# Optimization experiments

Measured on AMD Instinct MI355X. Metric: run time of the kernel, lower is better.

The kernel has to match this reference:

```python
import jax, jax.numpy as jnp
import numpy as np
import math

DIM = 128
HEAD = 4
RANK = 32
HEAD_DIM = DIM // HEAD
B, T, N, F = 2, 128, 1024, 128  # t == f == dim required by the original module
EXPAND = 4
EPS = 1e-6


def setup_inputs() -> dict:
    key = jax.random.key(0)
    ks = jax.random.split(key, 12)
    s = 0.02
    return {
        "x": jax.random.normal(ks[0], (B, T, N, F), jnp.float32),
        "norm_w": jnp.ones((DIM,), jnp.float32),
        "q_w": jax.random.normal(ks[1], (DIM, DIM), jnp.float32) * s,   # (out,in)
        "q_b": jnp.zeros((DIM,), jnp.float32),
        "key_p": jax.random.normal(ks[2], (RANK, HEAD, HEAD_DIM), jnp.float32),
        "v_w": jax.random.normal(ks[3], (DIM, DIM), jnp.float32) * s,
        "v_b": jnp.zeros((DIM,), jnp.float32),
        "alpha": jnp.full((HEAD, 1), math.log(9.0), jnp.float32),
        "beta": jnp.full((HEAD, 1), math.log(0.01), jnp.float32),
        "w1": jax.random.normal(ks[4], (EXPAND * DIM, DIM), jnp.float32) * s,
        "b1": jnp.zeros((EXPAND * DIM,), jnp.float32),
        "w2": jax.random.normal(ks[5], (EXPAND * DIM, DIM), jnp.float32) * s,
        "b2": jnp.zeros((EXPAND * DIM,), jnp.float32),
        "w3": jax.random.normal(ks[6], (DIM, EXPAND * DIM), jnp.float32) * s,
        "b3": jnp.zeros((DIM,), jnp.float32),
    }


def _rmsnorm(x, w):
    # NOTE: original reduces over axis 1 (the t axis), weight broadcasts on last axis
    var = jnp.mean(x * x, axis=1, keepdims=True)
    return w * (x * jax.lax.rsqrt(var + EPS))


def _attention(x, q_w, q_b, key_p, v_w, v_b, alpha, beta):
    b, t, n, f = x.shape
    q = (jnp.einsum('btnf,of->btno', x, q_w) + q_b).reshape(b, t, n, HEAD, HEAD_DIM)
    attn = jnp.einsum('btnhd,rhd->btnhr', q, key_p) / (HEAD_DIM ** 0.5)
    xv = (jnp.einsum('btnf,of->btno', x, v_w) + v_b).reshape(b, t, n, HEAD, HEAD_DIM)
    # softmax over rank, aggregate values into landmarks
    v = jnp.einsum('btnhr,btnhd->btrhd', jax.nn.softmax(attn, axis=-1), xv)
    # softmax over node axis (axis=-3 of btnhr), scatter landmarks back to nodes
    v = jnp.einsum('btnhr,btrhd->btnhd', jax.nn.softmax(attn, axis=-3), v)
    v = jax.nn.sigmoid(alpha) * xv + jax.nn.sigmoid(beta) * v
    return v.reshape(b, t, n, f)


def _conv1x1(x, w, b):
    # Conv2d kernel_size=1 on (B, C=t, H=n, W=f)
    return jnp.einsum('oc,bcnf->bonf', w, x) + b[None, :, None, None]


def _ffn(x, w1, b1, w2, b2, w3, b3):
    h = jax.nn.silu(_conv1x1(x, w1, b1)) * _conv1x1(x, w2, b2)
    return _conv1x1(h, w3, b3)  # dropout is identity in eval mode


def reference(x, norm_w, q_w, q_b, key_p, v_w, v_b, alpha, beta,
              w1, b1, w2, b2, w3, b3):
    x = _attention(_rmsnorm(x, norm_w), q_w, q_b, key_p, v_w, v_b, alpha, beta) + x
    x = _ffn(_rmsnorm(x, norm_w), w1, b1, w2, b2, w3, b3) + x
    return x
```

## Files before the change

kernel.cpp:

```cpp
#include <hip/hip_runtime.h>

#define DEV static __device__ __forceinline__

constexpr int Bc = 2, Tc = 128, Nc = 1024, Fc = 128, Hc = 4, Rc = 32, Dc = 32;
constexpr int NF  = Nc * Fc;
constexpr int TOK = Bc * Tc * Nc;
constexpr float EPSc = 1e-6f;
constexpr float RSD  = 0.17677669529663687f;

typedef __bf16 bf16x8 __attribute__((ext_vector_type(8)));
typedef float  f32x16 __attribute__((ext_vector_type(16)));
typedef unsigned short us8 __attribute__((ext_vector_type(8)));
typedef unsigned short us4 __attribute__((ext_vector_type(4)));

DEV unsigned short f2bu(float f) {
    unsigned u = __builtin_bit_cast(unsigned, f);
    u += 0x7fffu + ((u >> 16) & 1u);
    return (unsigned short)(u >> 16);
}
DEV float bu2f(unsigned short s) {
    return __builtin_bit_cast(float, ((unsigned)s) << 16);
}
DEV float sigmoidf_(float z) { return 1.f / (1.f + __expf(-z)); }
DEV f32x16 zero16() { f32x16 z;
#pragma unroll
    for (int i = 0; i < 16; i++) z[i] = 0.f;
    return z; }

__global__ void k_prep(const float* __restrict__ q_w, const float* __restrict__ q_b,
                       const float* __restrict__ key_p, const float* __restrict__ v_b,
                       const float* __restrict__ v_w,
                       unsigned short* __restrict__ Wcat, float* __restrict__ bias,
                       const float* __restrict__ w1, const float* __restrict__ w2,
                       const float* __restrict__ w3, unsigned short* __restrict__ wbf)
{
    __shared__ float sqw[32][128];
    __shared__ float skp[32][32];
    const int blk = blockIdx.x, tid = threadIdx.x;
    if (blk < 4) {
        int h = blk;
        for (int i = tid; i < 4096; i += 256) {
            int d = i >> 7, c = i & 127;
            sqw[d][c] = q_w[(size_t)(h * 32 + d) * 128 + c];
        }
        for (int i = tid; i < 1024; i += 256) {
            int r = i >> 5, d = i & 31;
            skp[r][d] = key_p[(size_t)(r * 4 + h) * 32 + d] * RSD;
        }
        __syncthreads();
        int r = tid >> 3;
        int c0 = (tid & 7) * 16;
        for (int cc = 0; cc < 16; ++cc) {
            int c = c0 + cc;
            float s = 0.f;
#pragma unroll
            for (int d = 0; d < 32; ++d) s = fmaf(sqw[d][c], skp[r][d], s);
            Wcat[(size_t)(h * 32 + r) * 128 + c] = f2bu(s);
        }
        if (tid < 32) {
            float s = 0.f;
#pragma unroll
            for (int d = 0; d < 32; ++d) s = fmaf(q_b[h * 32 + d], skp[tid][d], s);
            bias[h * 32 + tid] = s;
        }
        if (h == 0 && tid >= 64 && tid < 192) bias[128 + tid - 64] = v_b[tid - 64];
        return;
    }
    const float* src;
    unsigned short* dst;
    long i8;
    if (blk < 12) {
        i8 = (long)(blk - 4) * 2048 + tid * 8;
        src = v_w; dst = Wcat + 16384;
    } else {
        i8 = (long)(blk - 12) * 2048 + tid * 8;
        if (i8 < 65536)        { src = w1; dst = wbf; }
        else if (i8 < 131072)  { src = w2 - 65536; dst = wbf; }
        else                   { src = w3 - 131072; dst = wbf; }
    }
    float4 u0 = *(const float4*)(src + i8);
    float4 u1 = *(const float4*)(src + i8 + 4);
    us4 p0, p1;
    p0[0] = f2bu(u0.x); p0[1] = f2bu(u0.y); p0[2] = f2bu(u0.z); p0[3] = f2bu(u0.w);
    p1[0] = f2bu(u1.x); p1[1] = f2bu(u1.y); p1[2] = f2bu(u1.z); p1[3] = f2bu(u1.w);
    *(us4*)(dst + i8)     = p0;
    *(us4*)(dst + i8 + 4) = p1;
}

constexpr int XPF = 132;
__global__ __launch_bounds__(256, 2) void k_projm(
    const float* __restrict__ x, const float* __restrict__ nw,
    const unsigned short* __restrict__ Wcat, const float* __restrict__ bias,
    unsigned short* __restrict__ Lb, unsigned short* __restrict__ XVb)
{
    __shared__ float xs[128 * XPF];
    __shared__ float sscale[128];
    const int tid = threadIdx.x, lane = tid & 63, wv = tid >> 6;
    const int lr = lane & 31, lhi = lane >> 5;
    const int blk = blockIdx.x;
    const int b = blk >> 10, n = blk & 1023;

    const float* xg = x + ((size_t)(b * Tc) * Nc + n) * 128;
#pragma unroll
    for (int p = 0; p < 8; ++p) {
        int i = p * 256 + tid;
        int t = i >> 4, cg = i & 15;
        const float* src = xg + (size_t)t * NF + cg * 8;
        float4 u0 = *(const float4*)src;
        float4 u1 = *(const float4*)(src + 4);
        int col = t ^ ((cg & 7) << 3);
        float vv[8] = {u0.x, u0.y, u0.z, u0.w, u1.x, u1.y, u1.z, u1.w};
#pragma unroll
        for (int j = 0; j < 8; ++j) xs[(cg * 8 + j) * XPF + col] = vv[j];
    }
    __syncthreads();

    {
        int c = tid >> 1, half = tid & 1;
        float ss = 0.f;
#pragma unroll
        for (int k = 0; k < 16; ++k) {
            float4 u = *(const float4*)&xs[c * XPF + half * 64 + k * 4];
            ss = fmaf(u.x, u.x, fmaf(u.y, u.y, fmaf(u.z, u.z, fmaf(u.w, u.w, ss))));
        }
        ss += __shfl_xor(ss, 1);
        if (half == 0) sscale[c] = rsqrtf(ss * (1.f / Tc) + EPSc) * nw[c];
    }
    __syncthreads();

    bf16x8 af[8];
#pragma unroll
    for (int s = 0; s < 8; ++s) {
        const int cbase = s * 16 + lhi * 8;
        const int col = (wv * 32 + lr) ^ (((cbase >> 3) & 7) << 3);
        bf16x8 v;
#pragma unroll
        for (int j = 0; j < 8; ++j) {
            const int c = cbase + j;
            v[j] = (__bf16)(xs[c * XPF + col] * sscale[c]);
        }
        af[s] = v;
    }

#pragma unroll
    for (int ot = 0; ot < 8; ++ot) {
        const unsigned short* pw = Wcat + (size_t)(ot * 32 + lr) * 128 + lhi * 8;
        f32x16 acc = zero16();
#pragma unroll
        for (int s = 0; s < 8; ++s) {
            bf16x8 bw = *(const bf16x8*)(pw + s * 16);
            acc = __builtin_amdgcn_mfma_f32_32x32x16_bf16(af[s], bw, acc, 0, 0, 0);
        }
        const int o = ot * 32 + lr;
        const float bv = bias[o];
        unsigned short* dst = (ot < 4) ? Lb : XVb;
        const int oo = (ot < 4) ? o : o - 128;
#pragma unroll
        for (int r = 0; r < 16; ++r) {
            const int t = wv * 32 + (r & 3) + 8 * (r >> 2) + 4 * lhi;
            dst[((size_t)(b * Tc + t) * Nc + n) * 128 + oo] = f2bu(acc[r] + bv);
        }
    }
}

__global__ __launch_bounds__(256, 4) void k_land(
    const unsigned short* __restrict__ Lb, const unsigned short* __restrict__ XVb,
    float* __restrict__ VL, float* __restrict__ M2, float* __restrict__ S2)
{
    __shared__ float sL [64][34];
    __shared__ float sXV[64][36];
    __shared__ float redm[32][8];
    __shared__ float reds[32][8];
    int tid = threadIdx.x;
    int blk = blockIdx.x;
    int h = blk & 3; int bt = blk >> 2;
    size_t base = (size_t)bt * Nc * 128 + h * 32;
    const int li = tid >> 2, c8 = (tid & 3) * 8;
    const int r_st = tid & 31, stripe = tid >> 5;
    const int ti = tid >> 2, sub = tid & 3;
    const int r_acc = tid >> 3, d0 = (tid & 7) * 4;
    float m_st = -1e30f, s_st = 0.f;
    float a0 = 0, a1 = 0, a2 = 0, a3 = 0;
    for (int n0 = 0; n0 < Nc; n0 += 64) {
        {
            size_t g = base + (size_t)(n0 + li) * 128 + c8;
            us8 vL = *(const us8*)(Lb + g);
            us8 vX = *(const us8*)(XVb + g);
#pragma unroll
            for (int j = 0; j < 8; ++j) {
                sL [li][c8 + j] = bu2f(vL[j]);
                sXV[li][c8 + j] = bu2f(vX[j]);
            }
        }
        __syncthreads();
#pragma unroll
        for (int i8 = 0; i8 < 8; ++i8) {
            float v = sL[stripe * 8 + i8][r_st];
            float mn = fmaxf(m_st, v);
            s_st = s_st * __expf(m_st - mn) + __expf(v - mn);
            m_st = mn;
        }
        float e[8];
        float mx = -1e30f;
#pragma unroll
        for (int j = 0; j < 8; ++j) mx = fmaxf(mx, sL[ti][sub * 8 + j]);
        mx = fmaxf(mx, __shfl_xor(mx, 1));
        mx = fmaxf(mx, __shfl_xor(mx, 2));
        float sm = 0.f;
#pragma unroll
        for (int j = 0; j < 8; ++j) { e[j] = __expf(sL[ti][sub * 8 + j] - mx); sm += e[j]; }
        sm += __shfl_xor(sm, 1);
        sm += __shfl_xor(sm, 2);
        float iv = 1.f / sm;
        __syncthreads();
#pragma unroll
        for (int j = 0; j < 8; ++j) sL[ti][sub * 8 + j] = e[j] * iv;
        __syncthreads();
#pragma unroll 2
        for (int i = 0; i < 64; ++i) {
            float p = sL[i][r_acc];
            float4 v = *(const float4*)&sXV[i][d0];
            a0 = fmaf(p, v.x, a0); a1 = fmaf(p, v.y, a1);
            a2 = fmaf(p, v.z, a2); a3 = fmaf(p, v.w, a3);
        }
        __syncthreads();
    }
    redm[r_st][stripe] = m_st;
    reds[r_st][stripe] = s_st;
    __syncthreads();
    if (tid < 32) {
        float m = -1e30f;
#pragma unroll
        for (int k = 0; k < 8; ++k) m = fmaxf(m, redm[tid][k]);
        float s = 0.f;
#pragma unroll
        for (int k = 0; k < 8; ++k) s += reds[tid][k] * __expf(redm[tid][k] - m);
        M2[blk * 32 + tid] = m;
        S2[blk * 32 + tid] = s;
    }
    *(float4*)&VL[((size_t)blk * 32 + r_acc) * 32 + d0] = make_float4(a0, a1, a2, a3);
}

__global__ __launch_bounds__(256) void k_out1(
    const float* __restrict__ x,
    const unsigned short* __restrict__ Lb, const unsigned short* __restrict__ XVb,
    const float* __restrict__ VL, const float* __restrict__ M2, const float* __restrict__ S2,
    const float* __restrict__ alpha, const float* __restrict__ beta,
    unsigned short* __restrict__ X2b)
{
    __shared__ float sVL[128][32];
    __shared__ float sP[8][128];
    __shared__ float sM[128], sSi[128], sAB[8];
    int tid = threadIdx.x;
    int tk00 = blockIdx.x * 64;
    int bt = tk00 >> 10;
    for (int k = tid; k < 4096; k += 256) sVL[k >> 5][k & 31] = VL[(size_t)bt * 4096 + k];
    if (tid < 128) { sM[tid] = M2[bt * 128 + tid]; sSi[tid] = 1.f / S2[bt * 128 + tid]; }
    if (tid < 8)   sAB[tid] = (tid < 4) ? sigmoidf_(alpha[tid]) : sigmoidf_(beta[tid - 4]);
    __syncthreads();
    const int ti = tid >> 5, quad = tid & 31;
    const int h = quad >> 3, d0 = (quad & 7) * 4;
    const int hr0 = h * 32;
    const int f4 = (tid & 31) * 4;
    const float sa = sAB[h], sb = sAB[4 + h];
    for (int tg = 0; tg < 8; ++tg) {
        const int tk0 = tk00 + tg * 8;
        {
            us4 lv = *(const us4*)&Lb[(size_t)(tk0 + ti) * 128 + f4];
#pragma unroll
            for (int j = 0; j < 4; ++j)
                sP[ti][f4 + j] = __expf(bu2f(lv[j]) - sM[f4 + j]) * sSi[f4 + j];
        }
        __syncthreads();
        float a0 = 0, a1 = 0, a2 = 0, a3 = 0;
#pragma unroll 4
        for (int r = 0; r < 32; ++r) {
            float p = sP[ti][hr0 + r];
            float4 v = *(const float4*)&sVL[hr0 + r][d0];
            a0 = fmaf(p, v.x, a0); a1 = fmaf(p, v.y, a1);
            a2 = fmaf(p, v.z, a2); a3 = fmaf(p, v.w, a3);
        }
        size_t gi = (size_t)(tk0 + ti) * 128 + quad * 4;
        ushort4 xv4 = *(const ushort4*)&XVb[gi];
        float o0 = fmaf(sb, a0, fmaf(sa, bu2f(xv4.x), x[gi + 0]));
        float o1 = fmaf(sb, a1, fmaf(sa, bu2f(xv4.y), x[gi + 1]));
        float o2 = fmaf(sb, a2, fmaf(sa, bu2f(xv4.z), x[gi + 2]));
        float o3 = fmaf(sb, a3, fmaf(sa, bu2f(xv4.w), x[gi + 3]));
        ushort4 pk; pk.x = f2bu(o0); pk.y = f2bu(o1); pk.z = f2bu(o2); pk.w = f2bu(o3);
        *(ushort4*)&X2b[gi] = pk;
        __syncthreads();
    }
}

constexpr int XST = 132;
__global__ __launch_bounds__(256, 2) void k_ffn_mfma(
    const unsigned short* __restrict__ X2b, const float* __restrict__ nw,
    const unsigned short* __restrict__ w1b, const float* __restrict__ b1,
    const unsigned short* __restrict__ w2b, const float* __restrict__ b2,
    const unsigned short* __restrict__ w3b, const float* __restrict__ b3,
    float* __restrict__ out)
{
    __shared__ unsigned short smem[18432] __attribute__((aligned(16)));
    unsigned short* xstage = smem;
    unsigned short* gT     = smem;
    __shared__ float sscale[128];

    const int tid  = threadIdx.x;
    const int lane = tid & 63;
    const int wv   = tid >> 6;
    const int lr   = lane & 31;
    const int lhi  = lane >> 5;
    const int blk  = blockIdx.x;
    const int b    = blk >> 10, n = blk & 1023;

    const int mrow = (wv & 1) * 32;
    const int fh   = (wv >> 1) * 64;
    const int t0   = wv * 32;

    const unsigned short* xg = X2b + ((size_t)(b * Tc) * Nc + n) * 128;
#pragma unroll
    for (int p = 0; p < 8; ++p) {
        int i = p * 256 + tid;
        int t = i >> 4, fg = i & 15;
        us8 v = *(const us8*)(xg + (size_t)t * NF + fg * 8);
        int tt = t ^ ((fg & 7) << 3);
#pragma unroll
        for (int j = 0; j < 8; ++j) xstage[(fg * 8 + j) * XST + tt] = v[j];
    }
    __syncthreads();

    {
        int f = tid >> 1, half = tid & 1;
        float ss = 0.f;
#pragma unroll
        for (int kk = 0; kk < 16; ++kk) {
            us4 u = *(const us4*)&xstage[f * XST + half * 64 + kk * 4];
#pragma unroll
            for (int j = 0; j < 4; ++j) { float v = bu2f(u[j]); ss = fmaf(v, v, ss); }
        }
        ss += __shfl_xor(ss, 1);
        if (half == 0) sscale[f] = rsqrtf(ss * (1.f / Tc) + EPSc) * nw[f];
    }
    __syncthreads();

    bf16x8 xnf[2][8];
#pragma unroll
    for (int ft = 0; ft < 2; ++ft) {
        const int f = fh + ft * 32 + lr;
        const int swz = ((f >> 3) & 7) << 3;
        const float scale = sscale[f];
#pragma unroll
        for (int s = 0; s < 8; ++s) {
            int tb = (s * 16 + lhi * 8) ^ swz;
            us4 u0 = *(const us4*)&xstage[f * XST + tb];
            us4 u1 = *(const us4*)&xstage[f * XST + tb + 4];
            bf16x8 v;
#pragma unroll
            for (int j = 0; j < 4; ++j) {
                v[j]     = (__bf16)(bu2f(u0[j]) * scale);
                v[j + 4] = (__bf16)(bu2f(u1[j]) * scale);
            }
            xnf[ft][s] = v;
        }
    }

    f32x16 oacc[4];
#pragma unroll
    for (int c = 0; c < 4; ++c) {
        const int f = c * 32 + lr;
        const int swz = ((f >> 3) & 7) << 3;
#pragma unroll
        for (int q = 0; q < 4; ++q) {
            const int tb = t0 + 8 * q + 4 * lhi;
            us4 u = *(const us4*)&xstage[f * XST + (tb ^ swz)];
#pragma unroll
            for (int e = 0; e < 4; ++e)
                oacc[c][q * 4 + e] = bu2f(u[e]) + b3[tb + e];
        }
    }
    __syncthreads();

    const unsigned short* w1r = w1b + (size_t)(mrow + lr) * 128 + lhi * 8;
    const unsigned short* w2r = w2b + (size_t)(mrow + lr) * 128 + lhi * 8;
    const unsigned short* w3r = w3b + (size_t)(t0 + lr) * 512 + lhi * 8;

    int d = 0;
    for (int oc = 0; oc < 512; oc += 64) {
        bf16x8 a3[4];
        const unsigned short* pw3 = w3r + oc;
#pragma unroll
        for (int s = 0; s < 4; ++s) a3[s] = *(const bf16x8*)(pw3 + s * 16);

        f32x16 h1a = zero16(), h1b = zero16(), h2a = zero16(), h2b = zero16();
        const unsigned short* pw1 = w1r + (size_t)oc * 128;
        const unsigned short* pw2 = w2r + (size_t)oc * 128;
#pragma unroll
        for (int s = 0; s < 8; ++s) {
            bf16x8 a1 = *(const bf16x8*)(pw1 + s * 16);
            bf16x8 a2 = *(const bf16x8*)(pw2 + s * 16);
            h1a = __builtin_amdgcn_mfma_f32_32x32x16_bf16(a1, xnf[0][s], h1a, 0, 0, 0);
            h1b = __builtin_amdgcn_mfma_f32_32x32x16_bf16(a1, xnf[1][s], h1b, 0, 0, 0);
            h2a = __builtin_amdgcn_mfma_f32_32x32x16_bf16(a2, xnf[0][s], h2a, 0, 0, 0);
            h2b = __builtin_amdgcn_mfma_f32_32x32x16_bf16(a2, xnf[1][s], h2b, 0, 0, 0);
        }
        unsigned short* gTd = gT + d * 9216;
#pragma unroll
        for (int ft = 0; ft < 2; ++ft) {
            const int fcol = fh + ft * 32 + lr;
#pragma unroll
            for (int q = 0; q < 4; ++q) {
                ushort4 pk;
#pragma unroll
                for (int e = 0; e < 4; ++e) {
                    const int r = q * 4 + e;
                    const int orow = oc + mrow + e + 8 * q + 4 * lhi;
                    float z   = (ft ? h1b[r] : h1a[r]) + b1[orow];
                    float h2v = (ft ? h2b[r] : h2a[r]) + b2[orow];
                    float g   = z * sigmoidf_(z) * h2v;
                    unsigned short gb = f2bu(g);
                    if (e == 0) pk.x = gb; else if (e == 1) pk.y = gb;
                    else if (e == 2) pk.z = gb; else pk.w = gb;
                }
                const int o_l = mrow + 8 * q + 4 * lhi;
                *(ushort4*)&gTd[fcol * 72 + o_l] = pk;
            }
        }
        __syncthreads();
#pragma unroll
        for (int s = 0; s < 4; ++s) {
#pragma unroll
            for (int c = 0; c < 4; ++c) {
                bf16x8 bg = *(const bf16x8*)&gTd[(c * 32 + lr) * 72 + s * 16 + lhi * 8];
                oacc[c] = __builtin_amdgcn_mfma_f32_32x32x16_bf16(a3[s], bg, oacc[c], 0, 0, 0);
            }
        }
        d ^= 1;
    }

#pragma unroll
    for (int r = 0; r < 16; ++r) {
        const int t = t0 + (r & 3) + 8 * (r >> 2) + 4 * lhi;
        const size_t rowbase = ((size_t)(b * Tc + t) * Nc + n) * 128;
#pragma unroll
        for (int c = 0; c < 4; ++c) {
            out[rowbase + c * 32 + lr] = oacc[c][r];
        }
    }
}

extern "C" void kernel_launch(void* const* d_in, const int* in_sizes, int n_in,
                              void* d_out, int out_size, void* d_ws, size_t ws_size,
                              hipStream_t stream) {
    const float* x      = (const float*)d_in[0];
    const float* norm_w = (const float*)d_in[1];
    const float* q_w    = (const float*)d_in[2];
    const float* q_b    = (const float*)d_in[3];
    const float* key_p  = (const float*)d_in[4];
    const float* v_w    = (const float*)d_in[5];
    const float* v_b    = (const float*)d_in[6];
    const float* alpha  = (const float*)d_in[7];
    const float* beta   = (const float*)d_in[8];
    const float* w1     = (const float*)d_in[9];
    const float* b1     = (const float*)d_in[10];
    const float* w2     = (const float*)d_in[11];
    const float* b2     = (const float*)d_in[12];
    const float* w3     = (const float*)d_in[13];
    const float* b3     = (const float*)d_in[14];
    float* out = (float*)d_out;

    char* ws = (char*)d_ws;
    float* inv1 = (float*)ws;
    float* inv2 = inv1 + (size_t)Bc * NF;
    float* VLp  = inv2 + (size_t)Bc * NF;
    float* M2p  = VLp + (size_t)Bc * Tc * Hc * Rc * Dc;
    float* S2p  = M2p + (size_t)Bc * Tc * Hc * Rc;
    unsigned short* Lb  = (unsigned short*)(S2p + (size_t)Bc * Tc * Hc * Rc);
    unsigned short* XVb = Lb  + (size_t)TOK * 128;
    unsigned short* X2b = XVb + (size_t)TOK * 128;

    unsigned short* Wcat = (unsigned short*)VLp;
    float* bias256 = VLp + 16384;

    unsigned short* w1bf = (unsigned short*)inv2;
    unsigned short* w2bf = w1bf + 65536;
    unsigned short* w3bf = w1bf + 131072;

    k_prep    <<<108,           256, 0, stream>>>(q_w, q_b, key_p, v_b, v_w,
                                                  Wcat, bias256, w1, w2, w3, w1bf);
    k_projm   <<<Bc * Nc,       256, 0, stream>>>(x, norm_w, Wcat, bias256, Lb, XVb);
    k_land    <<<Bc * Tc * Hc,  256, 0, stream>>>(Lb, XVb, VLp, M2p, S2p);
    k_out1    <<<TOK / 64,      256, 0, stream>>>(x, Lb, XVb, VLp, M2p, S2p, alpha, beta, X2b);
    k_ffn_mfma<<<Bc * Nc,       256, 0, stream>>>(X2b, norm_w, w1bf, b1, w2bf, b2, w3bf, b3, out);
}
```

Measured before the change: 493.2 us.

## Repartition FFN waves by feature column and pass gate via lane shuffles

The FFN kernel's wave split changes. Each wave now owns 32 feature columns and computes all 64 hidden rows and all 128 output time steps for them, instead of splitting hidden rows and output rows across waves. Because each wave now produces its own gated activations, the LDS round trip and per-chunk __syncthreads for the hidden tile are replaced by in-register bf16 packing plus xor-32 lane shuffles that build the B operand for the second MFMA. Biases b1 and b2 are staged in LDS. In exchange each wave loads twice as many w1/w2 fragments and all of w3 per chunk, which increases global/L2 weight traffic and register pressure.

Result: slower. 675.1 us (+36.9%).

```diff
diff --git a/kernel.cpp b/kernel.cpp
--- a/kernel.cpp
+++ b/kernel.cpp
@@ -20,6 +20,9 @@
 }
 DEV float bu2f(unsigned short s) {
     return __builtin_bit_cast(float, ((unsigned)s) << 16);
+}
+DEV unsigned pk2(float lo, float hi) {
+    return (unsigned)f2bu(lo) | ((unsigned)f2bu(hi) << 16);
 }
 DEV float sigmoidf_(float z) { return 1.f / (1.f + __expf(-z)); }
 DEV f32x16 zero16() { f32x16 z;
@@ -300,10 +303,9 @@
     const unsigned short* __restrict__ w3b, const float* __restrict__ b3,
     float* __restrict__ out)
 {
-    __shared__ unsigned short smem[18432] __attribute__((aligned(16)));
-    unsigned short* xstage = smem;
-    unsigned short* gT     = smem;
+    __shared__ unsigned short xstage[128 * XST] __attribute__((aligned(16)));
     __shared__ float sscale[128];
+    __shared__ float sb1[512], sb2[512];
 
     const int tid  = threadIdx.x;
     const int lane = tid & 63;
@@ -312,10 +314,7 @@
     const int lhi  = lane >> 5;
     const int blk  = blockIdx.x;
     const int b    = blk >> 10, n = blk & 1023;
-
-    const int mrow = (wv & 1) * 32;
-    const int fh   = (wv >> 1) * 64;
-    const int t0   = wv * 32;
+    const int fcol = wv * 32 + lr;
 
     const unsigned short* xg = X2b + ((size_t)(b * Tc) * Nc + n) * 128;
 #pragma unroll
@@ -327,6 +326,8 @@
 #pragma unroll
         for (int j = 0; j < 8; ++j) xstage[(fg * 8 + j) * XST + tt] = v[j];
     }
+#pragma unroll
+    for (int i = tid; i < 512; i += 256) { sb1[i] = b1[i]; sb2[i] = b2[i]; }
     __syncthreads();
 
     {
@@ -343,107 +344,114 @@
     }
     __syncthreads();
 
-    bf16x8 xnf[2][8];
-#pragma unroll
-    for (int ft = 0; ft < 2; ++ft) {
-        const int f = fh + ft * 32 + lr;
-        const int swz = ((f >> 3) & 7) << 3;
-        const float scale = sscale[f];
+    bf16x8 xnf[8];
+    {
+        const int swz = ((fcol >> 3) & 7) << 3;
+        const float scale = sscale[fcol];
 #pragma unroll
         for (int s = 0; s < 8; ++s) {
             int tb = (s * 16 + lhi * 8) ^ swz;
-            us4 u0 = *(const us4*)&xstage[f * XST + tb];
-            us4 u1 = *(const us4*)&xstage[f * XST + tb + 4];
+            us4 u0 = *(const us4*)&xstage[fcol * XST + tb];
+            us4 u1 = *(const us4*)&xstage[fcol * XST + tb + 4];
             bf16x8 v;
 #pragma unroll
             for (int j = 0; j < 4; ++j) {
                 v[j]     = (__bf16)(bu2f(u0[j]) * scale);
                 v[j + 4] = (__bf16)(bu2f(u1[j]) * scale);
             }
-            xnf[ft][s] = v;
+            xnf[s] = v;
         }
     }
 
     f32x16 oacc[4];
+    {
+        const int swz = ((fcol >> 3) & 7) << 3;
+#pragma unroll
+        for (int c = 0; c < 4; ++c) {
+#pragma unroll
+            for (int q = 0; q < 4; ++q) {
+                const int tb = c * 32 + 8 * q + 4 * lhi;
+                us4 u = *(const us4*)&xstage[fcol * XST + (tb ^ swz)];
+#pragma unroll
+                for (int e = 0; e < 4; ++e)
+                    oacc[c][q * 4 + e] = bu2f(u[e]) + b3[tb + e];
+            }
+        }
+    }
+
+    for (int oc = 0; oc < 512; oc += 64) {
+        f32x16 h1a = zero16(), h1b = zero16(), h2a = zero16(), h2b = zero16();
+        const unsigned short* pw1a = w1b + (size_t)(oc + lr) * 128 + lhi * 8;
+        const unsigned short* pw2a = w2b + (size_t)(oc + lr) * 128 + lhi * 8;
+        const unsigned short* pw1b = pw1a + 32 * 128;
+        const unsigned short* pw2b = pw2a + 32 * 128;
+#pragma unroll
+        for (int s = 0; s < 8; ++s) {
+            bf16x8 a1a = *(const bf16x8*)(pw1a + s * 16);
+            bf16x8 a2a = *(const bf16x8*)(pw2a + s * 16);
+            bf16x8 a1b = *(const bf16x8*)(pw1b + s * 16);
+            bf16x8 a2b = *(const bf16x8*)(pw2b + s * 16);
+            h1a = __builtin_amdgcn_mfma_f32_32x32x16_bf16(a1a, xnf[s], h1a, 0, 0, 0);
+            h1b = __builtin_amdgcn_mfma_f32_32x32x16_bf16(a1b, xnf[s], h1b, 0, 0, 0);
+            h2a = __builtin_amdgcn_mfma_f32_32x32x16_bf16(a2a, xnf[s], h2a, 0, 0, 0);
+            h2b = __builtin_amdgcn_mfma_f32_32x32x16_bf16(a2b, xnf[s], h2b, 0, 0, 0);
+        }
+        unsigned P0[8], P1[8];
+#pragma unroll
+        for (int q = 0; q < 4; ++q) {
+            float4 b1a = *(const float4*)&sb1[oc + 8 * q + 4 * lhi];
+            float4 b2a = *(const float4*)&sb2[oc + 8 * q + 4 * lhi];
+            float4 b1bv = *(const float4*)&sb1[oc + 32 + 8 * q + 4 * lhi];
+            float4 b2bv = *(const float4*)&sb2[oc + 32 + 8 * q + 4 * lhi];
+            float ga[4], gb[4];
+#pragma unroll
+            for (int e = 0; e < 4; ++e) {
+                const int r = q * 4 + e;
+                float bb1a = (e == 0) ? b1a.x : (e == 1) ? b1a.y : (e == 2) ? b1a.z : b1a.w;
+                float bb2a = (e == 0) ? b2a.x : (e == 1) ? b2a.y : (e == 2) ? b2a.z : b2a.w;
+                float bb1b = (e == 0) ? b1bv.x : (e == 1) ? b1bv.y : (e == 2) ? b1bv.z : b1bv.w;
+                float bb2b = (e == 0) ? b2bv.x : (e == 1) ? b2bv.y : (e == 2) ? b2bv.z : b2bv.w;
+                float za = h1a[r] + bb1a;
+                ga[e] = za * sigmoidf_(za) * (h2a[r] + bb2a);
+                float zb = h1b[r] + bb1b;
+                gb[e] = zb * sigmoidf_(zb) * (h2b[r] + bb2b);
+            }
+            P0[2 * q]     = pk2(ga[0], ga[1]);
+            P0[2 * q + 1] = pk2(ga[2], ga[3]);
+            P1[2 * q]     = pk2(gb[0], gb[1]);
+            P1[2 * q + 1] = pk2(gb[2], gb[3]);
+        }
+#pragma unroll
+        for (int s = 0; s < 4; ++s) {
+            const int S4 = (s & 1) * 4;
+            unsigned o0, o1, o2, o3;
+            if (s >> 1) { o0 = P1[S4]; o1 = P1[S4 + 1]; o2 = P1[S4 + 2]; o3 = P1[S4 + 3]; }
+            else        { o0 = P0[S4]; o1 = P0[S4 + 1]; o2 = P0[S4 + 2]; o3 = P0[S4 + 3]; }
+            unsigned s0 = lhi ? o0 : o2;
+            unsigned s1 = lhi ? o1 : o3;
+            unsigned r0 = __shfl_xor(s0, 32, 64);
+            unsigned r1 = __shfl_xor(s1, 32, 64);
+            uint4 fr;
+            fr.x = lhi ? r0 : o0;
+            fr.y = lhi ? r1 : o1;
+            fr.z = lhi ? o2 : r0;
+            fr.w = lhi ? o3 : r1;
+            bf16x8 bg = __builtin_bit_cast(bf16x8, fr);
+#pragma unroll
+            for (int c = 0; c < 4; ++c) {
+                const unsigned short* pw3 = w3b + (size_t)(c * 32 + lr) * 512 + oc + s * 16 + lhi * 8;
+                bf16x8 a3 = *(const bf16x8*)pw3;
+                oacc[c] = __builtin_amdgcn_mfma_f32_32x32x16_bf16(a3, bg, oacc[c], 0, 0, 0);
+            }
+        }
+    }
+
 #pragma unroll
     for (int c = 0; c < 4; ++c) {
-        const int f = c * 32 + lr;
-        const int swz = ((f >> 3) & 7) << 3;
-#pragma unroll
-        for (int q = 0; q < 4; ++q) {
-            const int tb = t0 + 8 * q + 4 * lhi;
-            us4 u = *(const us4*)&xstage[f * XST + (tb ^ swz)];
-#pragma unroll
-            for (int e = 0; e < 4; ++e)
-                oacc[c][q * 4 + e] = bu2f(u[e]) + b3[tb + e];
-        }
-    }
-    __syncthreads();
-
-    const unsigned short* w1r = w1b + (size_t)(mrow + lr) * 128 + lhi * 8;
-    const unsigned short* w2r = w2b + (size_t)(mrow + lr) * 128 + lhi * 8;
-    const unsigned short* w3r = w3b + (size_t)(t0 + lr) * 512 + lhi * 8;
-
-    int d = 0;
-    for (int oc = 0; oc < 512; oc += 64) {
-        bf16x8 a3[4];
-        const unsigned short* pw3 = w3r + oc;
-#pragma unroll
-        for (int s = 0; s < 4; ++s) a3[s] = *(const bf16x8*)(pw3 + s * 16);
-
-        f32x16 h1a = zero16(), h1b = zero16(), h2a = zero16(), h2b = zero16();
-        const unsigned short* pw1 = w1r + (size_t)oc * 128;
-        const unsigned short* pw2 = w2r + (size_t)oc * 128;
-#pragma unroll
-        for (int s = 0; s < 8; ++s) {
-            bf16x8 a1 = *(const bf16x8*)(pw1 + s * 16);
-            bf16x8 a2 = *(const bf16x8*)(pw2 + s * 16);
-            h1a = __builtin_amdgcn_mfma_f32_32x32x16_bf16(a1, xnf[0][s], h1a, 0, 0, 0);
-            h1b = __builtin_amdgcn_mfma_f32_32x32x16_bf16(a1, xnf[1][s], h1b, 0, 0, 0);
-            h2a = __builtin_amdgcn_mfma_f32_32x32x16_bf16(a2, xnf[0][s], h2a, 0, 0, 0);
-            h2b = __builtin_amdgcn_mfma_f32_32x32x16_bf16(a2, xnf[1][s], h2b, 0, 0, 0);
-        }
-        unsigned short* gTd = gT + d * 9216;
-#pragma unroll
-        for (int ft = 0; ft < 2; ++ft) {
-            const int fcol = fh + ft * 32 + lr;
-#pragma unroll
-            for (int q = 0; q < 4; ++q) {
-                ushort4 pk;
-#pragma unroll
-                for (int e = 0; e < 4; ++e) {
-                    const int r = q * 4 + e;
-                    const int orow = oc + mrow + e + 8 * q + 4 * lhi;
-                    float z   = (ft ? h1b[r] : h1a[r]) + b1[orow];
-                    float h2v = (ft ? h2b[r] : h2a[r]) + b2[orow];
-                    float g   = z * sigmoidf_(z) * h2v;
-                    unsigned short gb = f2bu(g);
-                    if (e == 0) pk.x = gb; else if (e == 1) pk.y = gb;
-                    else if (e == 2) pk.z = gb; else pk.w = gb;
-                }
-                const int o_l = mrow + 8 * q + 4 * lhi;
-                *(ushort4*)&gTd[fcol * 72 + o_l] = pk;
-            }
-        }
-        __syncthreads();
-#pragma unroll
-        for (int s = 0; s < 4; ++s) {
-#pragma unroll
-            for (int c = 0; c < 4; ++c) {
-                bf16x8 bg = *(const bf16x8*)&gTd[(c * 32 + lr) * 72 + s * 16 + lhi * 8];
-                oacc[c] = __builtin_amdgcn_mfma_f32_32x32x16_bf16(a3[s], bg, oacc[c], 0, 0, 0);
-            }
-        }
-        d ^= 1;
-    }
-
-#pragma unroll
-    for (int r = 0; r < 16; ++r) {
-        const int t = t0 + (r & 3) + 8 * (r >> 2) + 4 * lhi;
-        const size_t rowbase = ((size_t)(b * Tc + t) * Nc + n) * 128;
-#pragma unroll
-        for (int c = 0; c < 4; ++c) {
-            out[rowbase + c * 32 + lr] = oacc[c][r];
+#pragma unroll
+        for (int r = 0; r < 16; ++r) {
+            const int t = c * 32 + (r & 3) + 8 * (r >> 2) + 4 * lhi;
+            out[((size_t)(b * Tc + t) * Nc + n) * 128 + fcol] = oacc[c][r];
         }
     }
 }
```
